# Kernel tuning notes

Measured on AMD Instinct MI355X. Metric: run time of the kernel, lower is better.

Reference implementation:

```python
import jax, jax.numpy as jnp
import numpy as np
import math

N, C_S, C_Z, C_IPA, H, NQ, NV = 768, 384, 128, 16, 12, 4, 8


def setup_inputs() -> dict:
    key = jax.random.key(0)
    ks = jax.random.split(key, 16)
    inp = {
        "s": jax.random.normal(ks[0], (N, C_S), jnp.float32),
        "z": jax.random.normal(ks[1], (N, N, C_Z), jnp.float32),
        "rots": jax.random.normal(ks[2], (N, 3, 3), jnp.float32),
        "trans": jax.random.normal(ks[3], (N, 3), jnp.float32),
        "mask": jnp.ones((N,), jnp.float32),
    }
    sc = 0.02
    inp["Wq"] = jax.random.normal(ks[4], (C_S, H * C_IPA), jnp.float32) * sc
    inp["bq"] = jnp.zeros((H * C_IPA,), jnp.float32)
    inp["Wkv"] = jax.random.normal(ks[5], (C_S, H * 2 * C_IPA), jnp.float32) * sc
    inp["bkv"] = jnp.zeros((H * 2 * C_IPA,), jnp.float32)
    inp["Wq3"] = jax.random.normal(ks[6], (C_S, H * 3 * NQ), jnp.float32) * sc
    inp["bq3"] = jnp.zeros((H * 3 * NQ,), jnp.float32)
    inp["Wkv3"] = jax.random.normal(ks[7], (C_S, H * 3 * (NQ + NV)), jnp.float32) * sc
    inp["bkv3"] = jnp.zeros((H * 3 * (NQ + NV),), jnp.float32)
    inp["Wb"] = jax.random.normal(ks[8], (C_Z, H), jnp.float32) * sc
    inp["bb"] = jnp.zeros((H,), jnp.float32)
    inp["hw"] = jnp.zeros((H,), jnp.float32)
    inp["Wo"] = jax.random.normal(ks[9], (H * (C_Z + C_IPA + NV * 4), C_S), jnp.float32) * sc
    inp["bo"] = jnp.zeros((C_S,), jnp.float32)
    return inp


def reference(s, z, rots, trans, mask, Wq, bq, Wkv, bkv, Wq3, bq3, Wkv3, bkv3, Wb, bb, hw, Wo, bo):
    normsize = math.sqrt(1.0 / (3 * C_IPA))
    normsize_B = math.sqrt(1.0 / 3.0)
    normsize_hw = math.sqrt(1.0 / (3 * NQ * 9.0 / 2))

    # scalar Q/K/V: [N, H, C_IPA]
    Q = (s @ Wq + bq).reshape(N, H, C_IPA)
    KV = (s @ Wkv + bkv).reshape(N, H, 2, C_IPA)
    K, V = KV[..., 0, :], KV[..., 1, :]

    # query points: project, place into global frame via rigid transform
    Q3 = (s @ Wq3 + bq3).reshape(N, 3, NQ * H).swapaxes(-1, -2)        # [N, NQ*H, 3]
    Q3 = jnp.einsum('nij,nkj->nki', rots, Q3) + trans[:, None, :]
    Q3 = Q3.reshape(N, H, NQ, 3)

    KV3 = (s @ Wkv3 + bkv3).reshape(N, 3, H * (NQ + NV)).swapaxes(-1, -2)
    KV3 = jnp.einsum('nij,nkj->nki', rots, KV3) + trans[:, None, :]
    KV3 = KV3.reshape(N, H, NQ + NV, 3)
    K3, V3 = KV3[:, :, :NQ, :], KV3[:, :, NQ:, :]                      # points per head

    # pair bias [N, N, H]
    B = z @ Wb + bb

    # scalar attention logits + pair bias
    AT = jnp.einsum('ihc,jhc->ijh', Q, K) * normsize + B * normsize_B

    # point attention: squared distances [N, N, H, NQ]
    d2 = jnp.sum(jnp.square(Q3[:, None] - K3[None, :]), axis=-1)
    hw_sp = jax.nn.softplus(hw) * normsize_hw                          # [H]
    AT3 = -0.5 * jnp.sum(d2 * hw_sp[None, None, :, None], axis=-1)     # [N, N, H]

    # mask bias: large negative where either residue masked out
    mask2 = mask[:, None] * mask[None, :]
    B3 = (mask2 - 1.0) * 1e9                                           # [N, N]

    AT = jax.nn.softmax(AT + AT3 + B3[..., None], axis=-2)             # softmax over j

    # scalar value aggregation
    O = jnp.einsum('ijh,jhc->ihc', AT, V).reshape(N, -1)

    # point value aggregation, then map back to local frame (inverse transform)
    O3 = jnp.einsum('ijh,jhcd->ihcd', AT, V3).reshape(N, H * NV, 3)
    O3 = jnp.einsum('nji,nkj->nki', rots, O3 - trans[:, None, :])      # rots^T @ (O3 - t)
    O3_norm = jnp.sqrt(jnp.sum(jnp.square(O3), axis=-1) + 1e-20)       # [N, H*NV]

    # pair representation aggregation
    O_pair = jnp.einsum('ijh,ijc->ihc', AT, z).reshape(N, -1)

    O_final = jnp.concatenate((O, O3[..., 0], O3[..., 1], O3[..., 2], O3_norm, O_pair), axis=-1)
    return O_final @ Wo + bo
```

## Files before the change

kernel.cpp:

```cpp
#include <hip/hip_runtime.h>
#include <cstdint>


typedef __attribute__((ext_vector_type(8))) short short8;
typedef __attribute__((ext_vector_type(4))) short short4_t;
typedef __attribute__((ext_vector_type(4))) float f32x4;

__device__ __forceinline__ unsigned short f2bf(float f) {
    unsigned u = __float_as_uint(f);
    u = (u + 0x7FFFu + ((u >> 16) & 1u)) >> 16;
    return (unsigned short)u;
}
__device__ __forceinline__ float bf2f(unsigned short s) {
    return __uint_as_float(((unsigned)s) << 16);
}
__device__ __forceinline__ unsigned pk2(float lo, float hi) {
    return (unsigned)f2bf(lo) | ((unsigned)f2bf(hi) << 16);
}
__device__ __forceinline__ int HOFF(int gg) {
    return gg * 6 + ((gg & 2) << 2);
}

#define NS_QK  0.14433756729740643f
#define NS_B   0.5773502691896258f
#define NS_HW  0.13608276348795434f

__global__ __launch_bounds__(256) void proj_kernel(
    const float* __restrict__ s,
    const float* __restrict__ Wq,   const float* __restrict__ bq,
    const float* __restrict__ Wkv,  const float* __restrict__ bkv,
    const float* __restrict__ Wq3,  const float* __restrict__ bq3,
    const float* __restrict__ Wkv3, const float* __restrict__ bkv3,
    float* __restrict__ Qw, unsigned short* __restrict__ Kw,
    unsigned short* __restrict__ Vt,
    float* __restrict__ P3q, float* __restrict__ P3kv)
{
    __shared__ __align__(16) float s_lds[32 * 384];
    const int t  = threadIdx.x;
    const int r0 = blockIdx.x * 32;
    const int c0 = blockIdx.y * 128;

    for (int u = t; u < 3072; u += 256) {
        int r = u / 96, c4 = u - r * 96;
        *(float4*)&s_lds[r * 384 + c4 * 4] =
            *(const float4*)&s[(size_t)(r0 + r) * 384 + c4 * 4];
    }
    __syncthreads();

    const int rg = t >> 6;
    const int lc = t & 63;
    const int colA = c0 + lc;
    const int colB = c0 + lc + 64;

    const float *wpA, *wpB; int ldA, ldB; float biasA, biasB;
    {
        int col = colA;
        if (col < 192)      { wpA = Wq   + col;       ldA = 192; biasA = bq[col]; }
        else if (col < 576) { wpA = Wkv  + (col-192); ldA = 384; biasA = bkv[col-192]; }
        else if (col < 720) { wpA = Wq3  + (col-576); ldA = 144; biasA = bq3[col-576]; }
        else                { wpA = Wkv3 + (col-720); ldA = 432; biasA = bkv3[col-720]; }
        col = colB;
        if (col < 192)      { wpB = Wq   + col;       ldB = 192; biasB = bq[col]; }
        else if (col < 576) { wpB = Wkv  + (col-192); ldB = 384; biasB = bkv[col-192]; }
        else if (col < 720) { wpB = Wq3  + (col-576); ldB = 144; biasB = bq3[col-576]; }
        else                { wpB = Wkv3 + (col-720); ldB = 432; biasB = bkv3[col-720]; }
    }

    float acc0[8] = {}, acc1[8] = {};
    for (int k = 0; k < 384; k += 4) {
        float4 sv[8];
        #pragma unroll
        for (int r = 0; r < 8; r++)
            sv[r] = *(const float4*)&s_lds[(rg*8 + r) * 384 + k];
        #pragma unroll
        for (int kk = 0; kk < 4; kk++) {
            float w0 = wpA[(k + kk) * ldA];
            float w1 = wpB[(k + kk) * ldB];
            #pragma unroll
            for (int r = 0; r < 8; r++) {
                float sval = ((const float*)&sv[r])[kk];
                acc0[r] += sval * w0;
                acc1[r] += sval * w1;
            }
        }
    }

    #pragma unroll
    for (int q = 0; q < 2; q++) {
        int col   = q ? colB : colA;
        float bia = q ? biasB : biasA;
        #pragma unroll
        for (int r = 0; r < 8; r++) {
            int row = r0 + rg*8 + r;
            float v = (q ? acc1[r] : acc0[r]) + bia;
            if (col < 192) {
                Qw[(size_t)row*192 + col] = v;
            } else if (col < 576) {
                int c = col - 192, h = c >> 5, sub = c & 31;
                if (sub < 16) Kw[(size_t)row*192 + h*16 + sub] = f2bf(v);
                else          Vt[(size_t)(h*16 + (sub-16))*768 + row] = f2bf(v);
            } else if (col < 720) {
                P3q[(size_t)row*144 + (col-576)] = v;
            } else {
                P3kv[(size_t)row*432 + (col-720)] = v;
            }
        }
    }
}

__global__ __launch_bounds__(192) void rot3_kernel(
    const float* __restrict__ P3q, const float* __restrict__ P3kv,
    const float* __restrict__ rots, const float* __restrict__ trans,
    float* __restrict__ Q3w, float* __restrict__ K3w,
    unsigned short* __restrict__ V3t)
{
    const int n = blockIdx.x;
    const int t = threadIdx.x;
    float R[9];
    #pragma unroll
    for (int u = 0; u < 9; u++) R[u] = rots[n*9 + u];
    float T0 = trans[n*3+0], T1 = trans[n*3+1], T2 = trans[n*3+2];

    float p0, p1, p2;
    if (t < 48) {
        p0 = P3q[(size_t)n*144 + t];
        p1 = P3q[(size_t)n*144 + 48 + t];
        p2 = P3q[(size_t)n*144 + 96 + t];
    } else {
        int k = t - 48;
        p0 = P3kv[(size_t)n*432 + k];
        p1 = P3kv[(size_t)n*432 + 144 + k];
        p2 = P3kv[(size_t)n*432 + 288 + k];
    }
    float o0 = R[0]*p0 + R[1]*p1 + R[2]*p2 + T0;
    float o1 = R[3]*p0 + R[4]*p1 + R[5]*p2 + T1;
    float o2 = R[6]*p0 + R[7]*p1 + R[8]*p2 + T2;

    if (t < 48) {
        Q3w[(size_t)n*144 + t*3 + 0] = o0;
        Q3w[(size_t)n*144 + t*3 + 1] = o1;
        Q3w[(size_t)n*144 + t*3 + 2] = o2;
    } else {
        int k = t - 48, h = k / 12, m = k % 12;
        if (m < 4) {
            size_t base = (size_t)n*144 + (h*4 + m)*3;
            K3w[base+0] = o0; K3w[base+1] = o1; K3w[base+2] = o2;
        } else {
            int rv = (h*8 + (m-4))*3;
            V3t[(size_t)(rv+0)*768 + n] = f2bf(o0);
            V3t[(size_t)(rv+1)*768 + n] = f2bf(o1);
            V3t[(size_t)(rv+2)*768 + n] = f2bf(o2);
        }
    }
}

__global__ __launch_bounds__(256) void ek_kernel(
    const float* __restrict__ Qw, const unsigned short* __restrict__ Kw,
    const float* __restrict__ Q3w, const float* __restrict__ K3w,
    const float* __restrict__ mask, const float* __restrict__ hw,
    const float* __restrict__ bb,
    unsigned short* __restrict__ EQw, unsigned short* __restrict__ EKw)
{
    const int idx = blockIdx.x * 4 + (threadIdx.x >> 6);
    const int h   = threadIdx.x & 63;
    if (h >= 12) return;
    const float hws = log1pf(__expf(hw[h])) * NS_HW;
    const float mi  = mask[idx];
    const float S   = 31616.0f;

    unsigned short row[32];
    {
        const unsigned short* kp = Kw + (size_t)idx*192 + h*16;
        #pragma unroll
        for (int c = 0; c < 16; c++) row[c] = kp[c];
        const float* k3 = K3w + (size_t)idx*144 + h*12;
        float kn = 0.0f;
        #pragma unroll
        for (int e = 0; e < 12; e++) {
            unsigned short b = f2bf(k3[e]);
            row[16+e] = b;
            float f = bf2f(b); kn += f*f;
        }
        row[28] = f2bf(bb[h]*NS_B - 0.5f*hws*kn);
        row[29] = f2bf(1.0f);
        row[30] = f2bf(mi * S);
        row[31] = f2bf(-S);
        unsigned short* o = EKw + ((size_t)idx*12 + h)*32;
        #pragma unroll
        for (int c = 0; c < 32; c++) o[c] = row[c];
    }
    {
        const float* qp = Qw + (size_t)idx*192 + h*16;
        #pragma unroll
        for (int c = 0; c < 16; c++) row[c] = f2bf(qp[c] * NS_QK);
        const float* q3 = Q3w + (size_t)idx*144 + h*12;
        float qn = 0.0f;
        #pragma unroll
        for (int e = 0; e < 12; e++) {
            float f = q3[e];
            row[16+e] = f2bf(f * hws);
            qn += f*f;
        }
        row[28] = f2bf(1.0f);
        row[29] = f2bf(-0.5f*hws*qn);
        row[30] = f2bf(mi * S);
        row[31] = f2bf(S);
        unsigned short* o = EQw + ((size_t)idx*12 + h)*32;
        #pragma unroll
        for (int c = 0; c < 32; c++) o[c] = row[c];
    }
}

__global__ __launch_bounds__(256, 3) void ipa_main(
    const float* __restrict__ z,
    const float* __restrict__ Wb,
    const unsigned short* __restrict__ EQw, const unsigned short* __restrict__ EKw,
    const unsigned short* __restrict__ Vt, const unsigned short* __restrict__ V3t,
    float* __restrict__ part3)
{
    __shared__ __align__(16) unsigned short z_l[90 * 88];
    __shared__ __align__(16) float          p_l[32 * 17];
    __shared__ __align__(16) unsigned short pT_l[16 * 40];
    __shared__ __align__(16) float          zb_l[32 * 13];
    __shared__ __align__(16) float          eq_l[12 * 33];
    __shared__ __align__(16) unsigned short wbT_l[16 * 136];

    const int i     = blockIdx.x >> 1;
    const int chunk = blockIdx.x & 1;
    const int t    = threadIdx.x;
    const int lane = t & 63;
    const int wv   = t >> 6;
    const int g    = lane >> 4;
    const int lm   = lane & 15;

    for (int u = t; u < 384; u += 256) {
        int h = u >> 5, c = u & 31;
        eq_l[h*33 + c] = bf2f(EQw[((size_t)i*12 + h)*32 + c]);
    }
    for (int u = t; u < 1536; u += 256) {
        int h = u % 12, c = u / 12;
        wbT_l[h*136 + c] = f2bf(Wb[c*12 + h]);
    }
    for (int u = t; u < 512; u += 256)
        wbT_l[(12 + (u >> 7))*136 + (u & 127)] = 0;
    if (t < 160) pT_l[480 + t] = 0;

    const int jj  = t >> 3, c16 = t & 7;
    const float* zbase = z + ((size_t)i*768 + chunk*384 + jj)*128 + c16*16;
    const int chS  = (jj >> 2)*8 + c16;
    const int chP  = chS + HOFF(chS >> 4);
    const int sidx = chP*88 + (jj & 3)*16;

    const unsigned short* rp1 = (t < 192)
        ? Vt + (size_t)t*768 : V3t + (size_t)(t - 192)*768;
    const int h1 = (t < 192) ? (t >> 4) : ((t - 192) / 24);
    const bool has2 = (t < 224);
    const unsigned short* rp2 = V3t + (size_t)(t + 64)*768;
    const int h2 = (t + 64) / 24;
    const int denh = (t >= 224 && t < 236) ? (t - 224) : -1;

    f32x4 opA = {0,0,0,0}, opB = {0,0,0,0};
    float acc1 = 0, acc2 = 0, dn = 0;

    {
        float4 f0 = *(const float4*)(zbase + 0);
        float4 f1 = *(const float4*)(zbase + 4);
        float4 f2 = *(const float4*)(zbase + 8);
        float4 f3 = *(const float4*)(zbase + 12);
        uint4* dst = (uint4*)&z_l[sidx];
        dst[0] = uint4{pk2(f0.x,f0.y), pk2(f0.z,f0.w), pk2(f1.x,f1.y), pk2(f1.z,f1.w)};
        dst[1] = uint4{pk2(f2.x,f2.y), pk2(f2.z,f2.w), pk2(f3.x,f3.y), pk2(f3.z,f3.w)};
    }
    __syncthreads();

    for (int tile = 0; tile < 12; tile++) {
        const int j0  = chunk*384 + tile*32;
        const bool more = (tile < 11);

        float4 zf0, zf1, zf2, zf3;
        if (more) {
            const float* zp = zbase + (size_t)(tile + 1) * 4096;
            zf0 = *(const float4*)(zp + 0);
            zf1 = *(const float4*)(zp + 4);
            zf2 = *(const float4*)(zp + 8);
            zf3 = *(const float4*)(zp + 12);
        }

        if (wv < 2) {
            f32x4 ab = {0,0,0,0};
            #pragma unroll
            for (int ks = 0; ks < 4; ks++) {
                short8 bf = *(const short8*)&wbT_l[lm*136 + ks*32 + g*8];
                int jr = wv*16 + lm;
                int ch = (jr >> 2)*8 + ks*2 + (g >> 1);
                int cp = ch + HOFF(ch >> 4);
                short8 a = *(const short8*)&z_l[cp*88 + (jr & 3)*16 + (g & 1)*8];
                ab = __builtin_amdgcn_mfma_f32_16x16x32_bf16(a, bf, ab, 0, 0, 0);
            }
            if (lm < 12) {
                #pragma unroll
                for (int r = 0; r < 4; r++)
                    zb_l[(wv*16 + g*4 + r)*13 + lm] = ab[r];
            }
        }
        __syncthreads();

        {
            auto b2item = [&](int id) {
                int jq = (id * 21846) >> 18;
                int h  = id - jq*12;
                float Bv = zb_l[jq*13 + h];
                const float* eqh = eq_l + h*33;
                const unsigned short* ek = EKw + ((size_t)(j0 + jq)*12 + h)*32;
                short8 e0 = *(const short8*)(ek);
                short8 e1 = *(const short8*)(ek + 8);
                short8 e2 = *(const short8*)(ek + 16);
                short8 e3 = *(const short8*)(ek + 24);
                float acc = Bv * NS_B;
                #pragma unroll
                for (int c = 0; c < 8; c++) acc += eqh[c]      * bf2f((unsigned short)e0[c]);
                #pragma unroll
                for (int c = 0; c < 8; c++) acc += eqh[8 + c]  * bf2f((unsigned short)e1[c]);
                #pragma unroll
                for (int c = 0; c < 8; c++) acc += eqh[16 + c] * bf2f((unsigned short)e2[c]);
                #pragma unroll
                for (int c = 0; c < 6; c++) acc += eqh[24 + c] * bf2f((unsigned short)e3[c]);
                float mterm = eqh[30] * bf2f((unsigned short)e3[6]);
                mterm += eqh[31] * bf2f((unsigned short)e3[7]);
                acc += mterm;
                float p = __expf(acc);
                p_l[jq*17 + h]  = p;
                pT_l[h*40 + jq] = f2bf(p);
            };
            b2item(t);
            if (t >= 128) b2item(t + 128);
        }
        __syncthreads();

        {
            const int nt0 = wv*2;
            short8 ap = *(const short8*)((const char*)pT_l + lm*80 + g*16);
            short8 b0, b1;
            #pragma unroll
            for (int e = 0; e < 8; e++) {
                int jje = g*8 + e;
                int su  = (jje >> 2)*8;
                int ro  = (jje & 3)*16;
                int cp0 = su + nt0 + HOFF(g);
                b0[e] = (short)z_l[cp0*88 + ro + lm];
                b1[e] = (short)z_l[(cp0 + 1)*88 + ro + lm];
            }
            opA = __builtin_amdgcn_mfma_f32_16x16x32_bf16(ap, b0, opA, 0, 0, 0);
            opB = __builtin_amdgcn_mfma_f32_16x16x32_bf16(ap, b1, opB, 0, 0, 0);
        }
        {
            const unsigned short* r1 = rp1 + j0;
            const unsigned short* r2 = rp2 + j0;
            #pragma unroll
            for (int q = 0; q < 4; q++) {
                short8 va = *(const short8*)(r1 + q*8);
                short8 vb;
                if (has2) vb = *(const short8*)(r2 + q*8);
                #pragma unroll
                for (int e = 0; e < 8; e++) {
                    int j2 = q*8 + e;
                    acc1 += p_l[j2*17 + h1] * bf2f((unsigned short)va[e]);
                    if (has2) acc2 += p_l[j2*17 + h2] * bf2f((unsigned short)vb[e]);
                }
            }
            if (denh >= 0) {
                #pragma unroll
                for (int j2 = 0; j2 < 32; j2++) dn += p_l[j2*17 + denh];
            }
        }

        uint4 s0, s1;
        if (more) {
            s0 = uint4{pk2(zf0.x,zf0.y), pk2(zf0.z,zf0.w), pk2(zf1.x,zf1.y), pk2(zf1.z,zf1.w)};
            s1 = uint4{pk2(zf2.x,zf2.y), pk2(zf2.z,zf2.w), pk2(zf3.x,zf3.y), pk2(zf3.z,zf3.w)};
        }
        __syncthreads();

        if (more) {
            uint4* dst = (uint4*)&z_l[sidx];
            dst[0] = s0; dst[1] = s1;
        }
        __syncthreads();
    }

    float* pb = part3 + (size_t)blockIdx.x * 2560;
    pb[t] = acc1;
    if (has2) pb[t + 256] = acc2;
    if (denh >= 0) pb[2304 + denh] = dn;
    {
        const int nt0 = wv*2;
        #pragma unroll
        for (int r = 0; r < 4; r++) {
            int h = g*4 + r;
            if (h < 12) {
                pb[768 + h*128 + nt0*16 + lm]       = opA[r];
                pb[768 + h*128 + (nt0 + 1)*16 + lm] = opB[r];
            }
        }
    }
}

__global__ __launch_bounds__(256) void combine_kernel(
    const float* __restrict__ part3, const float* __restrict__ rots,
    const float* __restrict__ trans, unsigned short* __restrict__ OF)
{
    const int i = blockIdx.x;
    const int t = threadIdx.x;
    const float* pa = part3 + (size_t)i*2*2560;
    const float* pb = pa + 2560;
    __shared__ float den_s[12];
    if (t < 12) den_s[t] = pa[2304 + t] + pb[2304 + t];
    __syncthreads();

    const size_t ofb = (size_t)i * 2112;
    if (t < 192) OF[ofb + t] = f2bf((pa[t] + pb[t]) / den_s[t >> 4]);
    if (t < 96) {
        int h = t >> 3, v = t & 7;
        float den = den_s[h];
        int base = 192 + t*3;
        float m0 = (pa[base+0] + pb[base+0]) / den - trans[i*3+0];
        float m1 = (pa[base+1] + pb[base+1]) / den - trans[i*3+1];
        float m2 = (pa[base+2] + pb[base+2]) / den - trans[i*3+2];
        const float* R = rots + (size_t)i*9;
        float r0v = R[0]*m0 + R[3]*m1 + R[6]*m2;
        float r1v = R[1]*m0 + R[4]*m1 + R[7]*m2;
        float r2v = R[2]*m0 + R[5]*m1 + R[8]*m2;
        float nrm = sqrtf(r0v*r0v + r1v*r1v + r2v*r2v + 1e-20f);
        int hv = h*8 + v;
        OF[ofb + 192 + hv] = f2bf(r0v);
        OF[ofb + 288 + hv] = f2bf(r1v);
        OF[ofb + 384 + hv] = f2bf(r2v);
        OF[ofb + 480 + hv] = f2bf(nrm);
    }
    for (int u = t; u < 1536; u += 256) {
        OF[ofb + 576 + u] = f2bf((pa[768 + u] + pb[768 + u]) / den_s[u >> 7]);
    }
}

__global__ __launch_bounds__(256) void out_gemm(
    const unsigned short* __restrict__ OF, const float* __restrict__ Wo,
    float* __restrict__ part)
{
    __shared__ __align__(16) float aT[32 * 132];
    __shared__ __align__(16) float bt[32 * 68];
    const int t  = threadIdx.x;
    const int i0 = blockIdx.x * 128;
    const int c0 = blockIdx.y * 64;
    const int k0 = blockIdx.z * 352;
    const int r0 = (t & 15) * 8;
    const int c4 = (t >> 4) * 4;

    float acc[8][4] = {};

    for (int kt = 0; kt < 11; kt++) {
        const int kk0 = k0 + kt*32;
        __syncthreads();
        {
            int r = t >> 1, kh = (t & 1) * 16;
            const unsigned short* apg = OF + (size_t)(i0 + r)*2112 + kk0 + kh;
            short8 v0 = *(const short8*)apg;
            short8 v1 = *(const short8*)(apg + 8);
            #pragma unroll
            for (int e = 0; e < 8; e++) aT[(kh + e)*132 + r]     = bf2f((unsigned short)v0[e]);
            #pragma unroll
            for (int e = 0; e < 8; e++) aT[(kh + 8 + e)*132 + r] = bf2f((unsigned short)v1[e]);
        }
        {
            int k = t >> 3, c8 = (t & 7) * 8;
            const float* wpg = Wo + (size_t)(kk0 + k)*384 + c0 + c8;
            *(float4*)&bt[k*68 + c8]     = *(const float4*)wpg;
            *(float4*)&bt[k*68 + c8 + 4] = *(const float4*)(wpg + 4);
        }
        __syncthreads();
        #pragma unroll 4
        for (int kk = 0; kk < 32; kk++) {
            float4 a0 = *(float4*)&aT[kk*132 + r0];
            float4 a1 = *(float4*)&aT[kk*132 + r0 + 4];
            float4 bv = *(float4*)&bt[kk*68 + c4];
            #pragma unroll
            for (int ci = 0; ci < 4; ci++) {
                float b = ((const float*)&bv)[ci];
                acc[0][ci] += ((const float*)&a0)[0] * b;
                acc[1][ci] += ((const float*)&a0)[1] * b;
                acc[2][ci] += ((const float*)&a0)[2] * b;
                acc[3][ci] += ((const float*)&a0)[3] * b;
                acc[4][ci] += ((const float*)&a1)[0] * b;
                acc[5][ci] += ((const float*)&a1)[1] * b;
                acc[6][ci] += ((const float*)&a1)[2] * b;
                acc[7][ci] += ((const float*)&a1)[3] * b;
            }
        }
    }

    float* pbv = part + (size_t)blockIdx.z * 294912;
    #pragma unroll
    for (int ri = 0; ri < 8; ri++) {
        float4 o = {acc[ri][0], acc[ri][1], acc[ri][2], acc[ri][3]};
        *(float4*)&pbv[(size_t)(i0 + r0 + ri)*384 + c0 + c4] = o;
    }
}

__global__ __launch_bounds__(256) void reduce_out(
    const float* __restrict__ part, const float* __restrict__ bo,
    float* __restrict__ out)
{
    int idx = blockIdx.x * 256 + threadIdx.x;
    float v = bo[idx % 384];
    #pragma unroll
    for (int s = 0; s < 6; s++) v += part[(size_t)s * 294912 + idx];
    out[idx] = v;
}

extern "C" void kernel_launch(void* const* d_in, const int* in_sizes, int n_in,
                              void* d_out, int out_size, void* d_ws, size_t ws_size,
                              hipStream_t stream) {
    const float* s     = (const float*)d_in[0];
    const float* z     = (const float*)d_in[1];
    const float* rots  = (const float*)d_in[2];
    const float* trans = (const float*)d_in[3];
    const float* mask  = (const float*)d_in[4];
    const float* Wq    = (const float*)d_in[5];
    const float* bq    = (const float*)d_in[6];
    const float* Wkv   = (const float*)d_in[7];
    const float* bkv   = (const float*)d_in[8];
    const float* Wq3   = (const float*)d_in[9];
    const float* bq3   = (const float*)d_in[10];
    const float* Wkv3  = (const float*)d_in[11];
    const float* bkv3  = (const float*)d_in[12];
    const float* Wb    = (const float*)d_in[13];
    const float* bb    = (const float*)d_in[14];
    const float* hw    = (const float*)d_in[15];
    const float* Wo    = (const float*)d_in[16];
    const float* bo    = (const float*)d_in[17];
    float* out = (float*)d_out;

    char* ws = (char*)d_ws;
    float*          Qw   = (float*)(ws + 0);
    float*          Q3w  = (float*)(ws + 589824);
    unsigned short* Kw   = (unsigned short*)(ws + 1032192);
    unsigned short* Vt   = (unsigned short*)(ws + 1327104);
    float*          K3w  = (float*)(ws + 1622016);
    unsigned short* V3t  = (unsigned short*)(ws + 2064384);
    float*          P3q  = (float*)(ws + 2506752);
    float*          P3kv = (float*)(ws + 2949120);
    unsigned short* EQw  = (unsigned short*)(ws + 4276224);
    unsigned short* EKw  = (unsigned short*)(ws + 4866048);
    unsigned short* OF   = (unsigned short*)(ws + 5455872);
    float*          part3 = (float*)(ws + 8699904);
    float*          part  = (float*)(ws + 8699904);

    proj_kernel<<<dim3(24, 9), 256, 0, stream>>>(
        s, Wq, bq, Wkv, bkv, Wq3, bq3, Wkv3, bkv3, Qw, Kw, Vt, P3q, P3kv);
    rot3_kernel<<<768, 192, 0, stream>>>(P3q, P3kv, rots, trans, Q3w, K3w, V3t);
    ek_kernel<<<192, 256, 0, stream>>>(Qw, Kw, Q3w, K3w, mask, hw, bb, EQw, EKw);
    ipa_main<<<1536, 256, 0, stream>>>(z, Wb, EQw, EKw, Vt, V3t, part3);
    combine_kernel<<<768, 256, 0, stream>>>(part3, rots, trans, OF);
    out_gemm<<<dim3(6, 6, 6), 256, 0, stream>>>(OF, Wo, part);
    reduce_out<<<1152, 256, 0, stream>>>(part, bo, out);
}
```

Measured before the change: 311.5 us.

## Drop register prefetch of z tiles, raise occupancy, shrink LDS padding, split accumulators

Removes the register double-buffer that prefetched the next z tile, so each tile is now loaded and converted to bf16 at the start of its own iteration. Raises the launch-bounds occupancy hint from 3 to 5 blocks, so the extra warps hide global latency instead of software prefetch. The z LDS padding formula is simplified to shrink the array, and the dot-product and reduction loops use several partial accumulators to shorten dependency chains. The trade-off is exposed load latency within each block, a tighter register budget, and possibly more LDS bank conflicts from the simpler padding.

```diff
diff --git a/kernel.cpp b/kernel.cpp
--- a/kernel.cpp
+++ b/kernel.cpp
@@ -17,9 +17,7 @@
 __device__ __forceinline__ unsigned pk2(float lo, float hi) {
     return (unsigned)f2bf(lo) | ((unsigned)f2bf(hi) << 16);
 }
-__device__ __forceinline__ int HOFF(int gg) {
-    return gg * 6 + ((gg & 2) << 2);
-}
+__device__ __forceinline__ int HOFF(int gg) { return gg * 6; }
 
 #define NS_QK  0.14433756729740643f
 #define NS_B   0.5773502691896258f
@@ -211,14 +209,14 @@
     }
 }
 
-__global__ __launch_bounds__(256, 3) void ipa_main(
+__global__ __launch_bounds__(256, 5) void ipa_main(
     const float* __restrict__ z,
     const float* __restrict__ Wb,
     const unsigned short* __restrict__ EQw, const unsigned short* __restrict__ EKw,
     const unsigned short* __restrict__ Vt, const unsigned short* __restrict__ V3t,
     float* __restrict__ part3)
 {
-    __shared__ __align__(16) unsigned short z_l[90 * 88];
+    __shared__ __align__(16) unsigned short z_l[82 * 88];
     __shared__ __align__(16) float          p_l[32 * 17];
     __shared__ __align__(16) unsigned short pT_l[16 * 40];
     __shared__ __align__(16) float          zb_l[32 * 13];
@@ -262,29 +260,22 @@
     f32x4 opA = {0,0,0,0}, opB = {0,0,0,0};
     float acc1 = 0, acc2 = 0, dn = 0;
 
-    {
-        float4 f0 = *(const float4*)(zbase + 0);
-        float4 f1 = *(const float4*)(zbase + 4);
-        float4 f2 = *(const float4*)(zbase + 8);
-        float4 f3 = *(const float4*)(zbase + 12);
-        uint4* dst = (uint4*)&z_l[sidx];
-        dst[0] = uint4{pk2(f0.x,f0.y), pk2(f0.z,f0.w), pk2(f1.x,f1.y), pk2(f1.z,f1.w)};
-        dst[1] = uint4{pk2(f2.x,f2.y), pk2(f2.z,f2.w), pk2(f3.x,f3.y), pk2(f3.z,f3.w)};
-    }
     __syncthreads();
 
     for (int tile = 0; tile < 12; tile++) {
-        const int j0  = chunk*384 + tile*32;
-        const bool more = (tile < 11);
-
-        float4 zf0, zf1, zf2, zf3;
-        if (more) {
-            const float* zp = zbase + (size_t)(tile + 1) * 4096;
-            zf0 = *(const float4*)(zp + 0);
-            zf1 = *(const float4*)(zp + 4);
-            zf2 = *(const float4*)(zp + 8);
-            zf3 = *(const float4*)(zp + 12);
-        }
+        const int j0 = chunk*384 + tile*32;
+
+        {
+            const float* zp = zbase + (size_t)tile * 4096;
+            float4 f0 = *(const float4*)(zp + 0);
+            float4 f1 = *(const float4*)(zp + 4);
+            float4 f2 = *(const float4*)(zp + 8);
+            float4 f3 = *(const float4*)(zp + 12);
+            uint4* dst = (uint4*)&z_l[sidx];
+            dst[0] = uint4{pk2(f0.x,f0.y), pk2(f0.z,f0.w), pk2(f1.x,f1.y), pk2(f1.z,f1.w)};
+            dst[1] = uint4{pk2(f2.x,f2.y), pk2(f2.z,f2.w), pk2(f3.x,f3.y), pk2(f3.z,f3.w)};
+        }
+        __syncthreads();
 
         if (wv < 2) {
             f32x4 ab = {0,0,0,0};
@@ -316,18 +307,18 @@
                 short8 e1 = *(const short8*)(ek + 8);
                 short8 e2 = *(const short8*)(ek + 16);
                 short8 e3 = *(const short8*)(ek + 24);
-                float acc = Bv * NS_B;
-                #pragma unroll
-                for (int c = 0; c < 8; c++) acc += eqh[c]      * bf2f((unsigned short)e0[c]);
-                #pragma unroll
-                for (int c = 0; c < 8; c++) acc += eqh[8 + c]  * bf2f((unsigned short)e1[c]);
-                #pragma unroll
-                for (int c = 0; c < 8; c++) acc += eqh[16 + c] * bf2f((unsigned short)e2[c]);
-                #pragma unroll
-                for (int c = 0; c < 6; c++) acc += eqh[24 + c] * bf2f((unsigned short)e3[c]);
+                float a0 = Bv * NS_B, a1 = 0, a2 = 0, a3 = 0;
+                #pragma unroll
+                for (int c = 0; c < 8; c++) a0 += eqh[c]      * bf2f((unsigned short)e0[c]);
+                #pragma unroll
+                for (int c = 0; c < 8; c++) a1 += eqh[8 + c]  * bf2f((unsigned short)e1[c]);
+                #pragma unroll
+                for (int c = 0; c < 8; c++) a2 += eqh[16 + c] * bf2f((unsigned short)e2[c]);
+                #pragma unroll
+                for (int c = 0; c < 6; c++) a3 += eqh[24 + c] * bf2f((unsigned short)e3[c]);
                 float mterm = eqh[30] * bf2f((unsigned short)e3[6]);
                 mterm += eqh[31] * bf2f((unsigned short)e3[7]);
-                acc += mterm;
+                float acc = ((a0 + a1) + (a2 + a3)) + mterm;
                 float p = __expf(acc);
                 p_l[jq*17 + h]  = p;
                 pT_l[h*40 + jq] = f2bf(p);
@@ -356,34 +347,32 @@
         {
             const unsigned short* r1 = rp1 + j0;
             const unsigned short* r2 = rp2 + j0;
+            float s1a = 0, s1b = 0, s2a = 0, s2b = 0;
             #pragma unroll
             for (int q = 0; q < 4; q++) {
                 short8 va = *(const short8*)(r1 + q*8);
                 short8 vb;
                 if (has2) vb = *(const short8*)(r2 + q*8);
+                float pa = 0, pbv2 = 0;
                 #pragma unroll
                 for (int e = 0; e < 8; e++) {
                     int j2 = q*8 + e;
-                    acc1 += p_l[j2*17 + h1] * bf2f((unsigned short)va[e]);
-                    if (has2) acc2 += p_l[j2*17 + h2] * bf2f((unsigned short)vb[e]);
+                    pa   += p_l[j2*17 + h1] * bf2f((unsigned short)va[e]);
+                    if (has2) pbv2 += p_l[j2*17 + h2] * bf2f((unsigned short)vb[e]);
                 }
-            }
+                if (q & 1) { s1b += pa; s2b += pbv2; }
+                else       { s1a += pa; s2a += pbv2; }
+            }
+            acc1 += s1a + s1b;
+            if (has2) acc2 += s2a + s2b;
             if (denh >= 0) {
-                #pragma unroll
-                for (int j2 = 0; j2 < 32; j2++) dn += p_l[j2*17 + denh];
-            }
-        }
-
-        uint4 s0, s1;
-        if (more) {
-            s0 = uint4{pk2(zf0.x,zf0.y), pk2(zf0.z,zf0.w), pk2(zf1.x,zf1.y), pk2(zf1.z,zf1.w)};
-            s1 = uint4{pk2(zf2.x,zf2.y), pk2(zf2.z,zf2.w), pk2(zf3.x,zf3.y), pk2(zf3.z,zf3.w)};
-        }
-        __syncthreads();
-
-        if (more) {
-            uint4* dst = (uint4*)&z_l[sidx];
-            dst[0] = s0; dst[1] = s1;
+                float da = 0, db = 0;
+                #pragma unroll
+                for (int j2 = 0; j2 < 16; j2++) da += p_l[j2*17 + denh];
+                #pragma unroll
+                for (int j2 = 16; j2 < 32; j2++) db += p_l[j2*17 + denh];
+                dn += da + db;
+            }
         }
         __syncthreads();
     }
```

Measured after the change: 538.2 us. +72.8%, slower.
